# Optimization experiments

Hardware: AMD Instinct MI355X
Metric: run time of the kernel (lower is better)

## Reference

```python
import jax, jax.numpy as jnp
import numpy as np
from math import sqrt

LOCAL_WINDOW = 32
STRIDE = 64


def _sparse_mask(L):
    # L_Q == L_K path of DozerAttention:
    #  - local window: diagonals at offsets 0..local_window//2 (both signs)
    #  - strided: diagonals at offsets 0, stride+1, 2*(stride+1), ... (both signs)
    i = jnp.arange(L)[:, None]
    j = jnp.arange(L)[None, :]
    d = jnp.abs(i - j)
    local = d <= (LOCAL_WINDOW // 2)
    strided = (d % (STRIDE + 1)) == 0
    return (local | strided).astype(jnp.float32)  # [L, L]


def setup_inputs() -> dict:
    key = jax.random.key(0)
    B, L, H, D = 2, 2048, 8, 64
    kq, kk, kv = jax.random.split(key, 3)
    queries = jax.random.normal(kq, (B, L, H, D), dtype=jnp.float32)
    keys = jax.random.normal(kk, (B, L, H, D), dtype=jnp.float32)
    values = jax.random.normal(kv, (B, L, H, D), dtype=jnp.float32)
    # TriangularCausalMask: True above the diagonal -> masked with -inf
    causal = jnp.triu(jnp.ones((L, L), dtype=bool), k=1)
    attn_mask = jnp.broadcast_to(causal[None, None], (B, 1, L, L))
    return {"queries": queries, "keys": keys, "values": values, "attn_mask": attn_mask}


def reference(queries, keys, values, attn_mask):
    B, L, H, D = queries.shape
    scale = 1.0 / sqrt(D)
    sm = _sparse_mask(L)  # [L, L]
    # Original fills a zero-initialized dense score tensor only at selected key
    # columns per query row; equivalent to dense QK^T elementwise-masked by sm
    # (non-selected entries stay exactly 0, NOT -inf -- faithful quirk).
    scores = jnp.einsum('blhe,bshe->bhls', queries, keys) * sm  # [B,H,L,L]
    scores = jnp.where(attn_mask, -jnp.inf, scores)
    A = jax.nn.softmax(scale * scores, axis=-1)  # dropout p=0.0 in this config
    V = jnp.einsum('bhls,bshd->blhd', A, values)  # [B,L,H,D]
    return V
```

## Files before the change

kernel.cpp:

```cpp
#include <hip/hip_runtime.h>
#include <hip/hip_bf16.h>

#define B_ 2
#define L_ 2048
#define H_ 8
#define D_ 64
#define SP_ 65
#define NC_ 128
#define NH_ 16
#define RS_ 512

typedef __attribute__((ext_vector_type(8))) short bf16x8;
typedef __attribute__((ext_vector_type(16))) float f32x16;

static __device__ inline short f2bf(float x) {
    return __builtin_bit_cast(short, __float2bfloat16(x));
}

static __device__ inline bf16x8 ld8_bf16(const float* __restrict__ p) {
    float4 a = *(const float4*)p;
    float4 b = *(const float4*)(p + 4);
    bf16x8 r;
    r[0]=f2bf(a.x); r[1]=f2bf(a.y); r[2]=f2bf(a.z); r[3]=f2bf(a.w);
    r[4]=f2bf(b.x); r[5]=f2bf(b.y); r[6]=f2bf(b.z); r[7]=f2bf(b.w);
    return r;
}

static __device__ inline bf16x8 ones_frag() {
    bf16x8 r;
    short o = f2bf(1.f);
    #pragma unroll
    for (int t = 0; t < 8; ++t) r[t] = o;
    return r;
}

__global__ __launch_bounds__(256) void pre_k(const float* __restrict__ q,
                                             const float* __restrict__ kk,
                                             const float* __restrict__ v,
                                             float* __restrict__ csum1,
                                             float* __restrict__ csumH,
                                             float* __restrict__ pB,
                                             float* __restrict__ zB) {
    __shared__ float LDS[4608];
    int wib  = threadIdx.x >> 6;
    int lane = threadIdx.x & 63;
    int half = lane >> 5, ln = lane & 31;
    int blk  = blockIdx.x;

    if (blk < 260) {
        int us = blk * 4 + wib;
        int bh = us / SP_;
        int r  = us % SP_;
        int h = bh & 7, b = bh >> 3;
        const size_t base = (size_t)b * L_ * RS_ + (size_t)h * D_;
        float* Pw = LDS + wib * 1152;

        bf16x8 bv0[2], bv1[2];
        #pragma unroll
        for (int kb = 0; kb < 2; ++kb) {
            int k0 = kb * 16 + half * 8;
            #pragma unroll
            for (int jj = 0; jj < 8; ++jj) {
                int lv = r + SP_ * (k0 + jj);
                lv = lv > L_ - 1 ? L_ - 1 : lv;
                const float* vr = v + base + (size_t)lv * RS_;
                bv0[kb][jj] = f2bf(vr[ln]);
                bv1[kb][jj] = f2bf(vr[32 + ln]);
            }
        }

        int lq = r + SP_ * ln;
        int lqc = lq > L_ - 1 ? L_ - 1 : lq;
        const float* qrow = q  + base + (size_t)lqc * RS_;
        const float* krow = kk + base + (size_t)lqc * RS_;
        f32x16 acc = {};
        #pragma unroll
        for (int kb = 0; kb < 4; ++kb) {
            bf16x8 a  = ld8_bf16(qrow + kb * 16 + half * 8);
            bf16x8 bb = ld8_bf16(krow + kb * 16 + half * 8);
            acc = __builtin_amdgcn_mfma_f32_32x32x16_bf16(a, bb, acc, 0, 0, 0);
        }
        #pragma unroll
        for (int rg = 0; rg < 16; ++rg) {
            int m = (rg & 3) + 8 * (rg >> 2) + 4 * half;
            bool act = (ln < m) && (r + SP_ * m < L_);
            Pw[m * 36 + ln] = act ? (__expf(0.125f * acc[rg]) - 1.f) : 0.f;
        }
        __syncthreads();

        f32x16 p0 = {}; f32x16 p1 = {}; f32x16 po = {};
        bf16x8 ones = ones_frag();
        #pragma unroll
        for (int kb = 0; kb < 2; ++kb) {
            int k0 = kb * 16 + half * 8;
            const float* pr = &Pw[ln * 36 + k0];
            float4 x = *(const float4*)pr;
            float4 y = *(const float4*)(pr + 4);
            bf16x8 ap;
            ap[0]=f2bf(x.x); ap[1]=f2bf(x.y); ap[2]=f2bf(x.z); ap[3]=f2bf(x.w);
            ap[4]=f2bf(y.x); ap[5]=f2bf(y.y); ap[6]=f2bf(y.z); ap[7]=f2bf(y.w);
            p0 = __builtin_amdgcn_mfma_f32_32x32x16_bf16(ap, bv0[kb], p0, 0, 0, 0);
            p1 = __builtin_amdgcn_mfma_f32_32x32x16_bf16(ap, bv1[kb], p1, 0, 0, 0);
            po = __builtin_amdgcn_mfma_f32_32x32x16_bf16(ap, ones,    po, 0, 0, 0);
        }
        float* pBr = pB + (size_t)bh * L_ * D_;
        float* zBr = zB + (size_t)bh * L_;
        #pragma unroll
        for (int rg = 0; rg < 16; ++rg) {
            int m = (rg & 3) + 8 * (rg >> 2) + 4 * half;
            int l = r + SP_ * m;
            if (l < L_) {
                pBr[(size_t)l * D_ + ln]      = p0[rg];
                pBr[(size_t)l * D_ + 32 + ln] = p1[rg];
                if (ln == 0) zBr[l] = po[rg];
            }
        }
    } else {
        int uc = (blk - 260) * 4 + wib;
        int cH = uc & (NH_ - 1);
        int bh = uc >> 4;
        int h = bh & 7, b = bh >> 3;
        const float* vb = v + (size_t)(b * L_ + cH * 128) * RS_ + h * D_ + lane;
        float* c1p = csum1 + ((size_t)bh * NC_ + cH * 8) * D_ + lane;
        float hs = 0.f;
        #pragma unroll
        for (int c = 0; c < 8; ++c) {
            float s0 = 0.f, s1 = 0.f, s2 = 0.f, s3 = 0.f;
            #pragma unroll
            for (int l = 0; l < 16; l += 4) {
                s0 += vb[(c * 16 + l + 0) * RS_]; s1 += vb[(c * 16 + l + 1) * RS_];
                s2 += vb[(c * 16 + l + 2) * RS_]; s3 += vb[(c * 16 + l + 3) * RS_];
            }
            float s = (s0 + s1) + (s2 + s3);
            c1p[c * D_] = s;
            hs += s;
        }
        csumH[((size_t)bh * NH_ + cH) * D_ + lane] = hs;
    }
}

__global__ __launch_bounds__(256) void local_k(const float* __restrict__ q,
                                               const float* __restrict__ kk,
                                               const float* __restrict__ v,
                                               const float* __restrict__ csum1,
                                               const float* __restrict__ csumH,
                                               const float* __restrict__ pB,
                                               const float* __restrict__ zB,
                                               float* __restrict__ out) {
    __shared__ float LDS[4672];
    int wib  = threadIdx.x >> 6;
    int lane = threadIdx.x & 63;
    int half = lane >> 5, ln = lane & 31;
    int wid = (blockIdx.x & 7) * 64 + (blockIdx.x >> 3);

    int tb = wib >> 1;
    int hf = wib & 1;
    int team = wid * 2 + tb;
    int bh = team >> 6;
    int T  = (team & 63) << 5;
    int h = bh & 7, b = bh >> 3;
    const size_t base = (size_t)b * L_ * RS_ + (size_t)h * D_;
    float* Pw = LDS + tb * 2176;
    float* PF = LDS + 4352 + tb * 128;
    float* ZW = LDS + 4608 + tb * 32;
    int d0 = 32 * hf;

    bf16x8 bv[4];
    #pragma unroll
    for (int kb = 0; kb < 4; ++kb) {
        #pragma unroll
        for (int jj = 0; jj < 8; ++jj) {
            int jr = T - 16 + kb * 16 + half * 8 + jj;
            jr = jr < 0 ? 0 : (jr > L_ - 1 ? L_ - 1 : jr);
            bv[kb][jj] = f2bf(v[base + (size_t)jr * RS_ + d0 + ln]);
        }
    }

    const float* qrow = q + base + (size_t)(T + ln) * RS_;
    bf16x8 aq[4];
    #pragma unroll
    for (int kb = 0; kb < 4; ++kb) aq[kb] = ld8_bf16(qrow + kb * 16 + half * 8);

    int j = T - 16 + d0 + ln;
    j = j < 0 ? 0 : (j > L_ - 1 ? L_ - 1 : j);
    const float* krow = kk + base + (size_t)j * RS_;
    f32x16 acc = {};
    #pragma unroll
    for (int kb = 0; kb < 4; ++kb) {
        bf16x8 kf = ld8_bf16(krow + kb * 16 + half * 8);
        acc = __builtin_amdgcn_mfma_f32_32x32x16_bf16(aq[kb], kf, acc, 0, 0, 0);
    }

    #pragma unroll
    for (int r = 0; r < 16; ++r) {
        int m = (r & 3) + 8 * (r >> 2) + 4 * half;
        float w;
        if (hf == 0) {
            bool act = (ln >= m) && (ln <= m + 16) && (T - 16 + ln >= 0);
            w = act ? (__expf(0.125f * acc[r]) - 1.f) : 0.f;
            if ((m < 16) && (ln >= 16) && (ln <= m + 16)) w += 1.f;
        } else {
            bool act = (ln <= m - 16);
            w = act ? (__expf(0.125f * acc[r]) - 1.f) : 0.f;
            if ((m >= 16) && (ln <= m - 16)) w += 1.f;
        }
        Pw[m * 68 + d0 + ln] = w;
    }

    if (hf == 0) {
        int c1 = T >> 4;
        int nH = c1 >> 3, nR = c1 & 7;
        const float* csH = csumH + (size_t)bh * NH_ * D_ + lane;
        const float* cs1 = csum1 + ((size_t)bh * NC_ + (c1 & ~7)) * D_ + lane;
        float s0 = 0.f, s1 = 0.f, s2 = 0.f, s3 = 0.f;
        int cc = 0;
        for (; cc + 4 <= nH; cc += 4) {
            s0 += csH[(cc + 0) * D_]; s1 += csH[(cc + 1) * D_];
            s2 += csH[(cc + 2) * D_]; s3 += csH[(cc + 3) * D_];
        }
        for (; cc < nH; ++cc) s0 += csH[cc * D_];
        for (int t = 0; t < nR; ++t) {
            if (t & 1) s1 += cs1[t * D_]; else s2 += cs1[t * D_];
        }
        float P0 = (s0 + s1) + (s2 + s3);
        float P1 = P0 + csum1[((size_t)bh * NC_ + c1) * D_ + lane];
        PF[lane]      = P0;
        PF[64 + lane] = P1;
    }
    __syncthreads();

    const float* pBr = pB + (size_t)bh * L_ * D_;
    const float* zBr = zB + (size_t)bh * L_;
    float pbv[16], zbv[16];
    #pragma unroll
    for (int r = 0; r < 16; ++r) {
        int m = (r & 3) + 8 * (r >> 2) + 4 * half;
        int i = T + m;
        pbv[r] = pBr[(size_t)i * D_ + d0 + ln];
        zbv[r] = zBr[i];
    }

    f32x16 p = {}; f32x16 po = {};
    bf16x8 ones = ones_frag();
    #pragma unroll
    for (int kb = 0; kb < 4; ++kb) {
        int k0 = kb * 16 + half * 8;
        const float* pr = &Pw[ln * 68 + k0];
        float4 x = *(const float4*)pr;
        float4 y = *(const float4*)(pr + 4);
        bf16x8 ap;
        ap[0]=f2bf(x.x); ap[1]=f2bf(x.y); ap[2]=f2bf(x.z); ap[3]=f2bf(x.w);
        ap[4]=f2bf(y.x); ap[5]=f2bf(y.y); ap[6]=f2bf(y.z); ap[7]=f2bf(y.w);
        p = __builtin_amdgcn_mfma_f32_32x32x16_bf16(ap, bv[kb], p, 0, 0, 0);
        if (hf == 1)
            po = __builtin_amdgcn_mfma_f32_32x32x16_bf16(ap, ones, po, 0, 0, 0);
    }

    if (hf == 1) {
        #pragma unroll
        for (int r = 0; r < 16; ++r) {
            int m = (r & 3) + 8 * (r >> 2) + 4 * half;
            if (ln == 0) ZW[m] = po[r] - (float)((m & 15) + 1);
        }
    }
    __syncthreads();

    float Pf0 = PF[d0 + ln];
    float Pf1 = PF[64 + d0 + ln];
    #pragma unroll
    for (int r = 0; r < 16; ++r) {
        int m = (r & 3) + 8 * (r >> 2) + 4 * half;
        int i = T + m;
        float z   = ZW[m] + zbv[r] + (float)(i + 1);
        float num = p[r] + pbv[r] + (m < 16 ? Pf0 : Pf1);
        out[base + (size_t)i * RS_ + d0 + ln] = num / z;
    }
}

extern "C" void kernel_launch(void* const* d_in, const int* in_sizes, int n_in,
                              void* d_out, int out_size, void* d_ws, size_t ws_size,
                              hipStream_t stream) {
    const float* q = (const float*)d_in[0];
    const float* k = (const float*)d_in[1];
    const float* v = (const float*)d_in[2];
    float* out = (float*)d_out;

    float* csum1 = (float*)d_ws;
    float* pB    = csum1 + (size_t)B_ * H_ * NC_ * D_;
    float* zB    = pB    + (size_t)B_ * H_ * L_ * D_;
    float* csumH = zB    + (size_t)B_ * H_ * L_;

    pre_k<<<324, 256, 0, stream>>>(q, k, v, csum1, csumH, pB, zB);
    local_k<<<512, 256, 0, stream>>>(q, k, v, csum1, csumH, pB, zB, out);
}
```

Before: 108.9 us.

## Fuse producer and consumer kernels with a global atomic flag barrier

Merges the precompute kernel and the local attention kernel into one launch. Consumer blocks compute their local QK/PV part first, then spin on a global counter until all 324 producer blocks have finished before reading the prefix sums and strided partials. This removes one kernel launch gap and overlaps consumer work with producers. The cost is an added memset, spin-wait polling, and a deadlock risk if consumers occupy every slot before all producers are scheduled.

```diff
diff --git a/kernel.cpp b/kernel.cpp
--- a/kernel.cpp
+++ b/kernel.cpp
@@ -9,6 +9,7 @@
 #define NC_ 128
 #define NH_ 16
 #define RS_ 512
+#define NPROD 324u
 
 typedef __attribute__((ext_vector_type(8))) short bf16x8;
 typedef __attribute__((ext_vector_type(16))) float f32x16;
@@ -34,14 +35,27 @@
     return r;
 }
 
-__global__ __launch_bounds__(256) void pre_k(const float* __restrict__ q,
-                                             const float* __restrict__ kk,
-                                             const float* __restrict__ v,
-                                             float* __restrict__ csum1,
-                                             float* __restrict__ csumH,
-                                             float* __restrict__ pB,
-                                             float* __restrict__ zB) {
-    __shared__ float LDS[4608];
+static __device__ inline void wait_flag(unsigned* flag, int lane) {
+    unsigned done;
+    do {
+        unsigned f = 0;
+        if (lane == 0) f = atomicAdd(flag, 0u);
+        done = (unsigned)__shfl((int)f, 0);
+        if (done < NPROD) __builtin_amdgcn_s_sleep(2);
+    } while (done < NPROD);
+    __threadfence();
+}
+
+__global__ __launch_bounds__(256, 4) void dozer_k(const float* __restrict__ q,
+                                                  const float* __restrict__ kk,
+                                                  const float* __restrict__ v,
+                                                  float* __restrict__ csum1,
+                                                  float* __restrict__ csumH,
+                                                  float* __restrict__ pB,
+                                                  float* __restrict__ zB,
+                                                  float* __restrict__ out,
+                                                  unsigned* __restrict__ flag) {
+    __shared__ float LDS[4672];
     int wib  = threadIdx.x >> 6;
     int lane = threadIdx.x & 63;
     int half = lane >> 5, ln = lane & 31;
@@ -115,7 +129,9 @@
                 if (ln == 0) zBr[l] = po[rg];
             }
         }
-    } else {
+        __syncthreads();
+        if (threadIdx.x == 0) { __threadfence(); atomicAdd(flag, 1u); }
+    } else if (blk < 324) {
         int uc = (blk - 260) * 4 + wib;
         int cH = uc & (NH_ - 1);
         int bh = uc >> 4;
@@ -136,144 +152,134 @@
             hs += s;
         }
         csumH[((size_t)bh * NH_ + cH) * D_ + lane] = hs;
-    }
-}
-
-__global__ __launch_bounds__(256) void local_k(const float* __restrict__ q,
-                                               const float* __restrict__ kk,
-                                               const float* __restrict__ v,
-                                               const float* __restrict__ csum1,
-                                               const float* __restrict__ csumH,
-                                               const float* __restrict__ pB,
-                                               const float* __restrict__ zB,
-                                               float* __restrict__ out) {
-    __shared__ float LDS[4672];
-    int wib  = threadIdx.x >> 6;
-    int lane = threadIdx.x & 63;
-    int half = lane >> 5, ln = lane & 31;
-    int wid = (blockIdx.x & 7) * 64 + (blockIdx.x >> 3);
-
-    int tb = wib >> 1;
-    int hf = wib & 1;
-    int team = wid * 2 + tb;
-    int bh = team >> 6;
-    int T  = (team & 63) << 5;
-    int h = bh & 7, b = bh >> 3;
-    const size_t base = (size_t)b * L_ * RS_ + (size_t)h * D_;
-    float* Pw = LDS + tb * 2176;
-    float* PF = LDS + 4352 + tb * 128;
-    float* ZW = LDS + 4608 + tb * 32;
-    int d0 = 32 * hf;
-
-    bf16x8 bv[4];
-    #pragma unroll
-    for (int kb = 0; kb < 4; ++kb) {
-        #pragma unroll
-        for (int jj = 0; jj < 8; ++jj) {
-            int jr = T - 16 + kb * 16 + half * 8 + jj;
-            jr = jr < 0 ? 0 : (jr > L_ - 1 ? L_ - 1 : jr);
-            bv[kb][jj] = f2bf(v[base + (size_t)jr * RS_ + d0 + ln]);
-        }
-    }
-
-    const float* qrow = q + base + (size_t)(T + ln) * RS_;
-    bf16x8 aq[4];
-    #pragma unroll
-    for (int kb = 0; kb < 4; ++kb) aq[kb] = ld8_bf16(qrow + kb * 16 + half * 8);
-
-    int j = T - 16 + d0 + ln;
-    j = j < 0 ? 0 : (j > L_ - 1 ? L_ - 1 : j);
-    const float* krow = kk + base + (size_t)j * RS_;
-    f32x16 acc = {};
-    #pragma unroll
-    for (int kb = 0; kb < 4; ++kb) {
-        bf16x8 kf = ld8_bf16(krow + kb * 16 + half * 8);
-        acc = __builtin_amdgcn_mfma_f32_32x32x16_bf16(aq[kb], kf, acc, 0, 0, 0);
-    }
-
-    #pragma unroll
-    for (int r = 0; r < 16; ++r) {
-        int m = (r & 3) + 8 * (r >> 2) + 4 * half;
-        float w;
-        if (hf == 0) {
-            bool act = (ln >= m) && (ln <= m + 16) && (T - 16 + ln >= 0);
-            w = act ? (__expf(0.125f * acc[r]) - 1.f) : 0.f;
-            if ((m < 16) && (ln >= 16) && (ln <= m + 16)) w += 1.f;
-        } else {
-            bool act = (ln <= m - 16);
-            w = act ? (__expf(0.125f * acc[r]) - 1.f) : 0.f;
-            if ((m >= 16) && (ln <= m - 16)) w += 1.f;
-        }
-        Pw[m * 68 + d0 + ln] = w;
-    }
-
-    if (hf == 0) {
-        int c1 = T >> 4;
-        int nH = c1 >> 3, nR = c1 & 7;
-        const float* csH = csumH + (size_t)bh * NH_ * D_ + lane;
-        const float* cs1 = csum1 + ((size_t)bh * NC_ + (c1 & ~7)) * D_ + lane;
-        float s0 = 0.f, s1 = 0.f, s2 = 0.f, s3 = 0.f;
-        int cc = 0;
-        for (; cc + 4 <= nH; cc += 4) {
-            s0 += csH[(cc + 0) * D_]; s1 += csH[(cc + 1) * D_];
-            s2 += csH[(cc + 2) * D_]; s3 += csH[(cc + 3) * D_];
-        }
-        for (; cc < nH; ++cc) s0 += csH[cc * D_];
-        for (int t = 0; t < nR; ++t) {
-            if (t & 1) s1 += cs1[t * D_]; else s2 += cs1[t * D_];
-        }
-        float P0 = (s0 + s1) + (s2 + s3);
-        float P1 = P0 + csum1[((size_t)bh * NC_ + c1) * D_ + lane];
-        PF[lane]      = P0;
-        PF[64 + lane] = P1;
-    }
-    __syncthreads();
-
-    const float* pBr = pB + (size_t)bh * L_ * D_;
-    const float* zBr = zB + (size_t)bh * L_;
-    float pbv[16], zbv[16];
-    #pragma unroll
-    for (int r = 0; r < 16; ++r) {
-        int m = (r & 3) + 8 * (r >> 2) + 4 * half;
-        int i = T + m;
-        pbv[r] = pBr[(size_t)i * D_ + d0 + ln];
-        zbv[r] = zBr[i];
-    }
-
-    f32x16 p = {}; f32x16 po = {};
-    bf16x8 ones = ones_frag();
-    #pragma unroll
-    for (int kb = 0; kb < 4; ++kb) {
-        int k0 = kb * 16 + half * 8;
-        const float* pr = &Pw[ln * 68 + k0];
-        float4 x = *(const float4*)pr;
-        float4 y = *(const float4*)(pr + 4);
-        bf16x8 ap;
-        ap[0]=f2bf(x.x); ap[1]=f2bf(x.y); ap[2]=f2bf(x.z); ap[3]=f2bf(x.w);
-        ap[4]=f2bf(y.x); ap[5]=f2bf(y.y); ap[6]=f2bf(y.z); ap[7]=f2bf(y.w);
-        p = __builtin_amdgcn_mfma_f32_32x32x16_bf16(ap, bv[kb], p, 0, 0, 0);
-        if (hf == 1)
-            po = __builtin_amdgcn_mfma_f32_32x32x16_bf16(ap, ones, po, 0, 0, 0);
-    }
-
-    if (hf == 1) {
+        __syncthreads();
+        if (threadIdx.x == 0) { __threadfence(); atomicAdd(flag, 1u); }
+    } else {
+        int cb = blk - 324;
+        int wid = (cb & 7) * 64 + (cb >> 3);
+
+        int tb = wib >> 1;
+        int hf = wib & 1;
+        int team = wid * 2 + tb;
+        int bh = team >> 6;
+        int T  = (team & 63) << 5;
+        int h = bh & 7, b = bh >> 3;
+        const size_t base = (size_t)b * L_ * RS_ + (size_t)h * D_;
+        float* Pw = LDS + tb * 2176;
+        float* PF = LDS + 4352 + tb * 128;
+        float* ZW = LDS + 4608 + tb * 32;
+        int d0 = 32 * hf;
+
+        bf16x8 bv[4];
+        #pragma unroll
+        for (int kb = 0; kb < 4; ++kb) {
+            #pragma unroll
+            for (int jj = 0; jj < 8; ++jj) {
+                int jr = T - 16 + kb * 16 + half * 8 + jj;
+                jr = jr < 0 ? 0 : (jr > L_ - 1 ? L_ - 1 : jr);
+                bv[kb][jj] = f2bf(v[base + (size_t)jr * RS_ + d0 + ln]);
+            }
+        }
+
+        const float* qrow = q + base + (size_t)(T + ln) * RS_;
+        bf16x8 aq[4];
+        #pragma unroll
+        for (int kb = 0; kb < 4; ++kb) aq[kb] = ld8_bf16(qrow + kb * 16 + half * 8);
+
+        int j = T - 16 + d0 + ln;
+        j = j < 0 ? 0 : (j > L_ - 1 ? L_ - 1 : j);
+        const float* krow = kk + base + (size_t)j * RS_;
+        f32x16 acc = {};
+        #pragma unroll
+        for (int kb = 0; kb < 4; ++kb) {
+            bf16x8 kf = ld8_bf16(krow + kb * 16 + half * 8);
+            acc = __builtin_amdgcn_mfma_f32_32x32x16_bf16(aq[kb], kf, acc, 0, 0, 0);
+        }
+
         #pragma unroll
         for (int r = 0; r < 16; ++r) {
             int m = (r & 3) + 8 * (r >> 2) + 4 * half;
-            if (ln == 0) ZW[m] = po[r] - (float)((m & 15) + 1);
-        }
-    }
-    __syncthreads();
-
-    float Pf0 = PF[d0 + ln];
-    float Pf1 = PF[64 + d0 + ln];
-    #pragma unroll
-    for (int r = 0; r < 16; ++r) {
-        int m = (r & 3) + 8 * (r >> 2) + 4 * half;
-        int i = T + m;
-        float z   = ZW[m] + zbv[r] + (float)(i + 1);
-        float num = p[r] + pbv[r] + (m < 16 ? Pf0 : Pf1);
-        out[base + (size_t)i * RS_ + d0 + ln] = num / z;
+            float w;
+            if (hf == 0) {
+                bool act = (ln >= m) && (ln <= m + 16) && (T - 16 + ln >= 0);
+                w = act ? (__expf(0.125f * acc[r]) - 1.f) : 0.f;
+                if ((m < 16) && (ln >= 16) && (ln <= m + 16)) w += 1.f;
+            } else {
+                bool act = (ln <= m - 16);
+                w = act ? (__expf(0.125f * acc[r]) - 1.f) : 0.f;
+                if ((m >= 16) && (ln <= m - 16)) w += 1.f;
+            }
+            Pw[m * 68 + d0 + ln] = w;
+        }
+        __syncthreads();
+
+        f32x16 p = {}; f32x16 po = {};
+        bf16x8 ones = ones_frag();
+        #pragma unroll
+        for (int kb = 0; kb < 4; ++kb) {
+            int k0 = kb * 16 + half * 8;
+            const float* pr = &Pw[ln * 68 + k0];
+            float4 x = *(const float4*)pr;
+            float4 y = *(const float4*)(pr + 4);
+            bf16x8 ap;
+            ap[0]=f2bf(x.x); ap[1]=f2bf(x.y); ap[2]=f2bf(x.z); ap[3]=f2bf(x.w);
+            ap[4]=f2bf(y.x); ap[5]=f2bf(y.y); ap[6]=f2bf(y.z); ap[7]=f2bf(y.w);
+            p = __builtin_amdgcn_mfma_f32_32x32x16_bf16(ap, bv[kb], p, 0, 0, 0);
+            if (hf == 1)
+                po = __builtin_amdgcn_mfma_f32_32x32x16_bf16(ap, ones, po, 0, 0, 0);
+        }
+
+        wait_flag(flag, lane);
+
+        if (hf == 0) {
+            int c1 = T >> 4;
+            int nH = c1 >> 3, nR = c1 & 7;
+            const float* csH = csumH + (size_t)bh * NH_ * D_ + lane;
+            const float* cs1 = csum1 + ((size_t)bh * NC_ + (c1 & ~7)) * D_ + lane;
+            float s0 = 0.f, s1 = 0.f, s2 = 0.f, s3 = 0.f;
+            int cc = 0;
+            for (; cc + 4 <= nH; cc += 4) {
+                s0 += csH[(cc + 0) * D_]; s1 += csH[(cc + 1) * D_];
+                s2 += csH[(cc + 2) * D_]; s3 += csH[(cc + 3) * D_];
+            }
+            for (; cc < nH; ++cc) s0 += csH[cc * D_];
+            for (int t = 0; t < nR; ++t) {
+                if (t & 1) s1 += cs1[t * D_]; else s2 += cs1[t * D_];
+            }
+            float P0 = (s0 + s1) + (s2 + s3);
+            float P1 = P0 + csum1[((size_t)bh * NC_ + c1) * D_ + lane];
+            PF[lane]      = P0;
+            PF[64 + lane] = P1;
+        } else {
+            #pragma unroll
+            for (int r = 0; r < 16; ++r) {
+                int m = (r & 3) + 8 * (r >> 2) + 4 * half;
+                if (ln == 0) ZW[m] = po[r] - (float)((m & 15) + 1);
+            }
+        }
+
+        const float* pBr = pB + (size_t)bh * L_ * D_;
+        const float* zBr = zB + (size_t)bh * L_;
+        float pbv[16], zbv[16];
+        #pragma unroll
+        for (int r = 0; r < 16; ++r) {
+            int m = (r & 3) + 8 * (r >> 2) + 4 * half;
+            int i = T + m;
+            pbv[r] = pBr[(size_t)i * D_ + d0 + ln];
+            zbv[r] = zBr[i];
+        }
+        __syncthreads();
+
+        float Pf0 = PF[d0 + ln];
+        float Pf1 = PF[64 + d0 + ln];
+        #pragma unroll
+        for (int r = 0; r < 16; ++r) {
+            int m = (r & 3) + 8 * (r >> 2) + 4 * half;
+            int i = T + m;
+            float z   = ZW[m] + zbv[r] + (float)(i + 1);
+            float num = p[r] + pbv[r] + (m < 16 ? Pf0 : Pf1);
+            out[base + (size_t)i * RS_ + d0 + ln] = num / z;
+        }
     }
 }
 
@@ -289,7 +295,8 @@
     float* pB    = csum1 + (size_t)B_ * H_ * NC_ * D_;
     float* zB    = pB    + (size_t)B_ * H_ * L_ * D_;
     float* csumH = zB    + (size_t)B_ * H_ * L_;
-
-    pre_k<<<324, 256, 0, stream>>>(q, k, v, csum1, csumH, pB, zB);
-    local_k<<<512, 256, 0, stream>>>(q, k, v, csum1, csumH, pB, zB, out);
-}
+    unsigned* flag = (unsigned*)(csumH + (size_t)B_ * H_ * NH_ * D_);
+
+    hipMemsetAsync(flag, 0, sizeof(unsigned), stream);
+    dozer_k<<<836, 256, 0, stream>>>(q, k, v, csum1, csumH, pB, zB, out, flag);
+}
```

New measurement: 177.9 us. 1.63x slower.
